# Optimization experiments

Measured on AMD Instinct MI355X. Metric: run time of the kernel, lower is better.

Reference implementation:

```python
import jax, jax.numpy as jnp
import numpy as np

B, H, S, D = 4, 16, 2048, 64
NEG = -9e15


def setup_inputs() -> dict:
    key = jax.random.key(0)
    kq, kk, kv = jax.random.split(key, 3)
    q = jax.random.normal(kq, (B, H, S, D), dtype=jnp.float32)
    k = jax.random.normal(kk, (B, H, S, D), dtype=jnp.float32)
    v = jax.random.normal(kv, (B, H, S, D), dtype=jnp.float32)
    # causal mask: 1 where attention allowed, 0 where masked
    mask = jnp.tril(jnp.ones((S, S), dtype=jnp.int32))[None, None]
    return {"q": q, "k": k, "v": v, "mask": mask}


def reference(q, k, v, mask):
    d_k = q.shape[-1]
    # [B,H,S,S] scores
    scores = jnp.einsum("bhqd,bhkd->bhqk", q, k) / jnp.sqrt(jnp.float32(d_k))
    scores = jnp.where(mask == 0, jnp.float32(NEG), scores)
    attn = jax.nn.softmax(scores, axis=-1)
    return jnp.einsum("bhqk,bhkd->bhqd", attn, v)
```

## Files before the change

kernel.cpp:

```cpp
#include <hip/hip_runtime.h>

#define SLEN 2048
#define DH 64
#define NH 64
#define KVB 64
#define NT 32
#define NP 16
#define NEGBIG (-1e30f)
#define SCALE 0.18033688011112042f

typedef __attribute__((ext_vector_type(8))) short bf16x8;
typedef __attribute__((ext_vector_type(8))) unsigned short u16x8;
typedef __attribute__((ext_vector_type(16))) float f32x16;
typedef __attribute__((ext_vector_type(4))) float f32x4;
typedef __attribute__((ext_vector_type(4))) unsigned int u32x4;

__device__ __forceinline__ ushort f2bf(float f) {
  union { float f; unsigned int u; } v; v.f = f;
  unsigned int r = v.u + 0x7fffu + ((v.u >> 16) & 1u);
  return (ushort)(r >> 16);
}

__device__ __forceinline__ unsigned int cvtpk(float lo, float hi2) {
  unsigned int r;
  asm("v_cvt_pk_bf16_f32 %0, %1, %2" : "=v"(r) : "v"(lo), "v"(hi2));
  return r;
}

__device__ __forceinline__ float xsumh(float x) { return x + __shfl_xor(x, 32); }

__device__ __forceinline__ void gload16(const ushort* g, ushort* l) {
  __builtin_amdgcn_global_load_lds(
      (const __attribute__((address_space(1))) void*)g,
      (__attribute__((address_space(3))) void*)l, 16, 0, 0);
}

__global__ __launch_bounds__(256) void prep_kv(const float* __restrict__ Kg,
                                               const float* __restrict__ Vg,
                                               ushort* __restrict__ wsK,
                                               ushort* __restrict__ wsV) {
  __shared__ float Vsh[KVB][DH + 1];
  const int head = blockIdx.x, tile = blockIdx.y, tid = threadIdx.x;
  const size_t goff = ((size_t)head * SLEN + (size_t)tile * KVB) * DH;
  const float* srcK = Kg + goff;
  const float* srcV = Vg + goff;
  ushort* dstK = wsK + ((size_t)head * NT + tile) * (KVB * DH);
  ushort* dstV = wsV + ((size_t)head * NT + tile) * (KVB * DH);
#pragma unroll
  for (int i = 0; i < 2; ++i) {
    const int id = tid + i * 256;
    const int r = id >> 3, c = id & 7;
    float4 a = *reinterpret_cast<const float4*>(srcK + r * DH + c * 8);
    float4 b = *reinterpret_cast<const float4*>(srcK + r * DH + c * 8 + 4);
    u16x8 t;
    t[0] = f2bf(a.x); t[1] = f2bf(a.y); t[2] = f2bf(a.z); t[3] = f2bf(a.w);
    t[4] = f2bf(b.x); t[5] = f2bf(b.y); t[6] = f2bf(b.z); t[7] = f2bf(b.w);
    *reinterpret_cast<u16x8*>(dstK + r * DH + ((c ^ (r & 7)) * 8)) = t;
  }
#pragma unroll
  for (int i = 0; i < 4; ++i) {
    const int n = tid + i * 256;
    const int row = n >> 4, c4 = (n & 15) << 2;
    *reinterpret_cast<float4*>(&Vsh[row][c4]) =
        *reinterpret_cast<const float4*>(srcV + row * DH + c4);
  }
  __syncthreads();
#pragma unroll
  for (int i = 0; i < 2; ++i) {
    const int id = tid + i * 256;
    const int d = id >> 3, c = id & 7;
    u16x8 t;
#pragma unroll
    for (int j = 0; j < 8; ++j) t[j] = f2bf(Vsh[c * 8 + j][d]);
    *reinterpret_cast<u16x8*>(dstV + d * DH + ((c ^ (d & 7)) * 8)) = t;
  }
}

__device__ __forceinline__ void qkt(const ushort* __restrict__ Kl,
                                    const bf16x8* qf, f32x16& s0, f32x16& s1,
                                    int ql, int hi) {
  s0 = (f32x16)0.0f; s1 = (f32x16)0.0f;
  __builtin_amdgcn_s_setprio(1);
#pragma unroll
  for (int ks = 0; ks < 4; ++ks) {
    const int c = ((ks * 2 + hi) ^ (ql & 7)) * 8;
    bf16x8 kf0 = *reinterpret_cast<const bf16x8*>(Kl + ql * 64 + c);
    bf16x8 kf1 = *reinterpret_cast<const bf16x8*>(Kl + (32 + ql) * 64 + c);
    s0 = __builtin_amdgcn_mfma_f32_32x32x16_bf16(kf0, qf[ks], s0, 0, 0, 0);
    s1 = __builtin_amdgcn_mfma_f32_32x32x16_bf16(kf1, qf[ks], s1, 0, 0, 0);
  }
  __builtin_amdgcn_s_setprio(0);
}

__device__ __forceinline__ void fin(const ushort* __restrict__ Vl,
                                    f32x16& s0, f32x16& s1, f32x16& o0,
                                    f32x16& o1, f32x4& lv, int t,
                                    int tl, int q0, int ql, int hi) {
  if (t == tl) {
    const int qg = q0 + ql;
#pragma unroll
    for (int r = 0; r < 16; ++r) {
      const int kr = t * 64 + (r & 3) + 8 * (r >> 2) + 4 * hi;
      if (kr > qg)      s0[r] = NEGBIG;
      if (kr + 32 > qg) s1[r] = NEGBIG;
    }
  }
#pragma unroll
  for (int r = 0; r < 16; ++r) s0[r] = __builtin_exp2f(s0[r]);
#pragma unroll
  for (int r = 0; r < 16; ++r) s1[r] = __builtin_exp2f(s1[r]);
#pragma unroll
  for (int r = 0; r < 16; ++r) lv[r & 3] += s0[r] + s1[r];

  unsigned int pw0[8], pw1[8];
#pragma unroll
  for (int g = 0; g < 4; ++g)
#pragma unroll
    for (int j = 0; j < 2; ++j) {
      pw0[g * 2 + j] = cvtpk(s0[4 * g + 2 * j], s0[4 * g + 2 * j + 1]);
      pw1[g * 2 + j] = cvtpk(s1[4 * g + 2 * j], s1[4 * g + 2 * j + 1]);
    }

  __builtin_amdgcn_s_setprio(1);
#pragma unroll
  for (int st = 0; st < 4; ++st) {
    const unsigned int* PW = (st < 2) ? pw0 : pw1;
    const int KH = st & 1;
    const unsigned int a0 = PW[4 * KH + 0], a1 = PW[4 * KH + 1];
    const unsigned int b0 = PW[4 * KH + 2], b1 = PW[4 * KH + 3];
    const unsigned int s0w = hi ? a0 : b0, s1w = hi ? a1 : b1;
    const unsigned int r0 = __shfl_xor(s0w, 32), r1 = __shfl_xor(s1w, 32);
    const unsigned int k0 = hi ? b0 : a0, k1 = hi ? b1 : a1;
    u32x4 fu;
    fu[0] = hi ? r0 : k0; fu[1] = hi ? r1 : k1;
    fu[2] = hi ? k0 : r0; fu[3] = hi ? k1 : r1;
    const bf16x8 pf = __builtin_bit_cast(bf16x8, fu);
    const int cv = ((st * 2 + hi) ^ (ql & 7)) * 8;
    const bf16x8 vf0 = *reinterpret_cast<const bf16x8*>(Vl + ql * 64 + cv);
    const bf16x8 vf1 = *reinterpret_cast<const bf16x8*>(Vl + (32 + ql) * 64 + cv);
    o0 = __builtin_amdgcn_mfma_f32_32x32x16_bf16(vf0, pf, o0, 0, 0, 0);
    o1 = __builtin_amdgcn_mfma_f32_32x32x16_bf16(vf1, pf, o1, 0, 0, 0);
  }
  __builtin_amdgcn_s_setprio(0);
}

__device__ __forceinline__ void load_q(const float* Qh, int q0, int ql, int hi,
                                       bf16x8* qf) {
  const float* qrow = Qh + (size_t)(q0 + ql) * DH;
#pragma unroll
  for (int ks = 0; ks < 4; ++ks) {
    const int d0 = ks * 16 + hi * 8;
    float4 a = *reinterpret_cast<const float4*>(qrow + d0);
    float4 b = *reinterpret_cast<const float4*>(qrow + d0 + 4);
    bf16x8 t;
    t[0] = (short)f2bf(a.x * SCALE); t[1] = (short)f2bf(a.y * SCALE);
    t[2] = (short)f2bf(a.z * SCALE); t[3] = (short)f2bf(a.w * SCALE);
    t[4] = (short)f2bf(b.x * SCALE); t[5] = (short)f2bf(b.y * SCALE);
    t[6] = (short)f2bf(b.z * SCALE); t[7] = (short)f2bf(b.w * SCALE);
    qf[ks] = t;
  }
}

__device__ __forceinline__ void epi(float* Ow, float* Oh, const f32x16& o,
                                    float invl, int q0, int subd, int lane) {
  const int ql = lane & 31, hi = lane >> 5;
#pragma unroll
  for (int g = 0; g < 4; ++g) {
    float4 vv = make_float4(o[4 * g] * invl, o[4 * g + 1] * invl,
                            o[4 * g + 2] * invl, o[4 * g + 3] * invl);
    *reinterpret_cast<float4*>(Ow + ql * 36 + 8 * g + 4 * hi) = vv;
  }
#pragma unroll
  for (int i = 0; i < 4; ++i) {
    const int qr = (lane >> 3) + i * 8;
    const int c4 = (lane & 7) * 4;
    float4 vv = *reinterpret_cast<const float4*>(Ow + qr * 36 + c4);
    *reinterpret_cast<float4*>(Oh + (size_t)(q0 + qr) * DH + subd * 32 + c4) = vv;
  }
}

__global__ __launch_bounds__(256, 4) void attn_fwd12(
    const float* __restrict__ Qg, const ushort* __restrict__ wsK,
    const ushort* __restrict__ wsV, float* __restrict__ Og) {
  __shared__ __align__(16) float smem[8192];
  ushort* stg = (ushort*)smem;

  const int head = blockIdx.x;
  const int p    = blockIdx.y;
  const int tid  = threadIdx.x;
  const int w    = tid >> 6;
  const int lane = tid & 63;
  const int hi   = lane >> 5;
  const int ql   = lane & 31;
  const int sel   = w & 1;
  const int which = w >> 1;

  const int q0 = (which ? (31 - p) : p) * 64 + sel * 32;
  const int tl = q0 >> 6;
  const int nt = 32 - p;

  const float*  Qh    = Qg + (size_t)head * SLEN * DH;
  float*        Oh    = Og + (size_t)head * SLEN * DH;
  const ushort* kbase = wsK + (size_t)head * (NT * KVB * DH);
  const ushort* vbase = wsV + (size_t)head * (NT * KVB * DH);

#define STAGE(buf, t)                                                          \
  do {                                                                         \
    const size_t tb_ = (size_t)(t) * 4096;                                     \
    _Pragma("unroll")                                                          \
    for (int j_ = 0; j_ < 2; ++j_) {                                           \
      gload16(kbase + tb_ + j_ * 2048 + tid * 8,                               \
              stg + (buf) * 8192 + j_ * 2048 + tid * 8);                       \
      gload16(vbase + tb_ + j_ * 2048 + tid * 8,                               \
              stg + (buf) * 8192 + 4096 + j_ * 2048 + tid * 8);                \
    }                                                                          \
  } while (0)

  STAGE(0, 0);

  bf16x8 qf[4];
  load_q(Qh, q0, ql, hi, qf);

  f32x16 o0 = (f32x16)0.0f, o1 = (f32x16)0.0f;
  f32x4 lv = (f32x4)0.0f;

  __syncthreads();

  int cur = 0;
  for (int t = 0; t < nt; ++t) {
    if (t + 1 < nt) STAGE(cur ^ 1, t + 1);

    if (t <= tl) {
      const ushort* Kl = stg + cur * 8192;
      const ushort* Vl = Kl + 4096;
      f32x16 s0, s1;
      qkt(Kl, qf, s0, s1, ql, hi);
      fin(Vl, s0, s1, o0, o1, lv, t, tl, q0, ql, hi);
    }
    __syncthreads();
    cur ^= 1;
  }
#undef STAGE

  const float ls = xsumh(lv[0] + lv[1] + lv[2] + lv[3]);

  float* Ow = smem + w * 1152;
  const float il = 1.0f / ls;
  epi(Ow, Oh, o0, il, q0, 0, lane);
  epi(Ow, Oh, o1, il, q0, 1, lane);
}

extern "C" void kernel_launch(void* const* d_in, const int* in_sizes, int n_in,
                              void* d_out, int out_size, void* d_ws, size_t ws_size,
                              hipStream_t stream) {
  const float* q = (const float*)d_in[0];
  const float* k = (const float*)d_in[1];
  const float* v = (const float*)d_in[2];
  float* out = (float*)d_out;

  const size_t per = (size_t)NH * SLEN * DH;
  ushort* wsK = (ushort*)d_ws;
  ushort* wsV = wsK + per;

  prep_kv<<<dim3(NH, NT), 256, 0, stream>>>(k, v, wsK, wsV);
  attn_fwd12<<<dim3(NH, NP), 256, 0, stream>>>(q, wsK, wsV, out);
}
```

Before: 95.74 us.

## Process two 32-row query tiles per wave to reuse K/V fragments

Each wave now handles a 64-row macro query tile (two 32-row halves), so every K and V fragment read from LDS feeds twice as many MFMAs. The grid is halved to 8 blocks per head, and each block's four waves take macro tiles b, 31-b, 8+b and 23-b, with the order reversed on odd heads to balance causal work. The goal is to cut LDS traffic and staging cost per unit of compute. In exchange, register pressure roughly doubles (launch bounds drop to 2 waves/SIMD occupancy) and the grid has fewer blocks.

```diff
diff --git a/kernel.cpp b/kernel.cpp
--- a/kernel.cpp
+++ b/kernel.cpp
@@ -5,7 +5,6 @@
 #define NH 64
 #define KVB 64
 #define NT 32
-#define NP 16
 #define NEGBIG (-1e30f)
 #define SCALE 0.18033688011112042f
 
@@ -76,72 +75,16 @@
   }
 }
 
-__device__ __forceinline__ void qkt(const ushort* __restrict__ Kl,
-                                    const bf16x8* qf, f32x16& s0, f32x16& s1,
-                                    int ql, int hi) {
-  s0 = (f32x16)0.0f; s1 = (f32x16)0.0f;
-  __builtin_amdgcn_s_setprio(1);
-#pragma unroll
-  for (int ks = 0; ks < 4; ++ks) {
-    const int c = ((ks * 2 + hi) ^ (ql & 7)) * 8;
-    bf16x8 kf0 = *reinterpret_cast<const bf16x8*>(Kl + ql * 64 + c);
-    bf16x8 kf1 = *reinterpret_cast<const bf16x8*>(Kl + (32 + ql) * 64 + c);
-    s0 = __builtin_amdgcn_mfma_f32_32x32x16_bf16(kf0, qf[ks], s0, 0, 0, 0);
-    s1 = __builtin_amdgcn_mfma_f32_32x32x16_bf16(kf1, qf[ks], s1, 0, 0, 0);
-  }
-  __builtin_amdgcn_s_setprio(0);
-}
-
-__device__ __forceinline__ void fin(const ushort* __restrict__ Vl,
-                                    f32x16& s0, f32x16& s1, f32x16& o0,
-                                    f32x16& o1, f32x4& lv, int t,
-                                    int tl, int q0, int ql, int hi) {
-  if (t == tl) {
-    const int qg = q0 + ql;
-#pragma unroll
-    for (int r = 0; r < 16; ++r) {
-      const int kr = t * 64 + (r & 3) + 8 * (r >> 2) + 4 * hi;
-      if (kr > qg)      s0[r] = NEGBIG;
-      if (kr + 32 > qg) s1[r] = NEGBIG;
-    }
-  }
-#pragma unroll
-  for (int r = 0; r < 16; ++r) s0[r] = __builtin_exp2f(s0[r]);
-#pragma unroll
-  for (int r = 0; r < 16; ++r) s1[r] = __builtin_exp2f(s1[r]);
-#pragma unroll
-  for (int r = 0; r < 16; ++r) lv[r & 3] += s0[r] + s1[r];
-
-  unsigned int pw0[8], pw1[8];
-#pragma unroll
-  for (int g = 0; g < 4; ++g)
-#pragma unroll
-    for (int j = 0; j < 2; ++j) {
-      pw0[g * 2 + j] = cvtpk(s0[4 * g + 2 * j], s0[4 * g + 2 * j + 1]);
-      pw1[g * 2 + j] = cvtpk(s1[4 * g + 2 * j], s1[4 * g + 2 * j + 1]);
-    }
-
-  __builtin_amdgcn_s_setprio(1);
-#pragma unroll
-  for (int st = 0; st < 4; ++st) {
-    const unsigned int* PW = (st < 2) ? pw0 : pw1;
-    const int KH = st & 1;
-    const unsigned int a0 = PW[4 * KH + 0], a1 = PW[4 * KH + 1];
-    const unsigned int b0 = PW[4 * KH + 2], b1 = PW[4 * KH + 3];
-    const unsigned int s0w = hi ? a0 : b0, s1w = hi ? a1 : b1;
-    const unsigned int r0 = __shfl_xor(s0w, 32), r1 = __shfl_xor(s1w, 32);
-    const unsigned int k0 = hi ? b0 : a0, k1 = hi ? b1 : a1;
-    u32x4 fu;
-    fu[0] = hi ? r0 : k0; fu[1] = hi ? r1 : k1;
-    fu[2] = hi ? k0 : r0; fu[3] = hi ? k1 : r1;
-    const bf16x8 pf = __builtin_bit_cast(bf16x8, fu);
-    const int cv = ((st * 2 + hi) ^ (ql & 7)) * 8;
-    const bf16x8 vf0 = *reinterpret_cast<const bf16x8*>(Vl + ql * 64 + cv);
-    const bf16x8 vf1 = *reinterpret_cast<const bf16x8*>(Vl + (32 + ql) * 64 + cv);
-    o0 = __builtin_amdgcn_mfma_f32_32x32x16_bf16(vf0, pf, o0, 0, 0, 0);
-    o1 = __builtin_amdgcn_mfma_f32_32x32x16_bf16(vf1, pf, o1, 0, 0, 0);
-  }
-  __builtin_amdgcn_s_setprio(0);
+__device__ __forceinline__ bf16x8 xchg(const unsigned int* PW, int KH, int hi) {
+  const unsigned int a0 = PW[4 * KH + 0], a1 = PW[4 * KH + 1];
+  const unsigned int b0 = PW[4 * KH + 2], b1 = PW[4 * KH + 3];
+  const unsigned int s0w = hi ? a0 : b0, s1w = hi ? a1 : b1;
+  const unsigned int r0 = __shfl_xor(s0w, 32), r1 = __shfl_xor(s1w, 32);
+  const unsigned int k0 = hi ? b0 : a0, k1 = hi ? b1 : a1;
+  u32x4 fu;
+  fu[0] = hi ? r0 : k0; fu[1] = hi ? r1 : k1;
+  fu[2] = hi ? k0 : r0; fu[3] = hi ? k1 : r1;
+  return __builtin_bit_cast(bf16x8, fu);
 }
 
 __device__ __forceinline__ void load_q(const float* Qh, int q0, int ql, int hi,
@@ -179,25 +122,31 @@
   }
 }
 
-__global__ __launch_bounds__(256, 4) void attn_fwd12(
+__global__ __launch_bounds__(256, 2) void attn_fwd13(
     const float* __restrict__ Qg, const ushort* __restrict__ wsK,
     const ushort* __restrict__ wsV, float* __restrict__ Og) {
   __shared__ __align__(16) float smem[8192];
   ushort* stg = (ushort*)smem;
 
   const int head = blockIdx.x;
-  const int p    = blockIdx.y;
+  const int b    = blockIdx.y;
   const int tid  = threadIdx.x;
   const int w    = tid >> 6;
   const int lane = tid & 63;
   const int hi   = lane >> 5;
   const int ql   = lane & 31;
-  const int sel   = w & 1;
-  const int which = w >> 1;
-
-  const int q0 = (which ? (31 - p) : p) * 64 + sel * 32;
-  const int tl = q0 >> 6;
-  const int nt = 32 - p;
+
+  const int wi = (head & 1) ? (3 - w) : w;
+  int macro;
+  if      (wi == 0) macro = b;
+  else if (wi == 1) macro = 31 - b;
+  else if (wi == 2) macro = 8 + b;
+  else              macro = 23 - b;
+
+  const int q0L = macro * 64;
+  const int q0U = macro * 64 + 32;
+  const int tl  = macro;
+  const int nt  = 32 - b;
 
   const float*  Qh    = Qg + (size_t)head * SLEN * DH;
   float*        Oh    = Og + (size_t)head * SLEN * DH;
@@ -218,11 +167,13 @@
 
   STAGE(0, 0);
 
-  bf16x8 qf[4];
-  load_q(Qh, q0, ql, hi, qf);
-
-  f32x16 o0 = (f32x16)0.0f, o1 = (f32x16)0.0f;
-  f32x4 lv = (f32x4)0.0f;
+  bf16x8 qfL[4], qfU[4];
+  load_q(Qh, q0L, ql, hi, qfL);
+  load_q(Qh, q0U, ql, hi, qfU);
+
+  f32x16 oL0 = (f32x16)0.0f, oL1 = (f32x16)0.0f;
+  f32x16 oU0 = (f32x16)0.0f, oU1 = (f32x16)0.0f;
+  f32x4 lvL = (f32x4)0.0f, lvU = (f32x4)0.0f;
 
   __syncthreads();
 
@@ -233,21 +184,89 @@
     if (t <= tl) {
       const ushort* Kl = stg + cur * 8192;
       const ushort* Vl = Kl + 4096;
-      f32x16 s0, s1;
-      qkt(Kl, qf, s0, s1, ql, hi);
-      fin(Vl, s0, s1, o0, o1, lv, t, tl, q0, ql, hi);
+
+      f32x16 sL0 = (f32x16)0.0f, sL1 = (f32x16)0.0f;
+      f32x16 sU0 = (f32x16)0.0f, sU1 = (f32x16)0.0f;
+      __builtin_amdgcn_s_setprio(1);
+#pragma unroll
+      for (int ks = 0; ks < 4; ++ks) {
+        const int c = ((ks * 2 + hi) ^ (ql & 7)) * 8;
+        const bf16x8 kf0 = *reinterpret_cast<const bf16x8*>(Kl + ql * 64 + c);
+        const bf16x8 kf1 =
+            *reinterpret_cast<const bf16x8*>(Kl + (32 + ql) * 64 + c);
+        sL0 = __builtin_amdgcn_mfma_f32_32x32x16_bf16(kf0, qfL[ks], sL0, 0, 0, 0);
+        sU0 = __builtin_amdgcn_mfma_f32_32x32x16_bf16(kf0, qfU[ks], sU0, 0, 0, 0);
+        sL1 = __builtin_amdgcn_mfma_f32_32x32x16_bf16(kf1, qfL[ks], sL1, 0, 0, 0);
+        sU1 = __builtin_amdgcn_mfma_f32_32x32x16_bf16(kf1, qfU[ks], sU1, 0, 0, 0);
+      }
+      __builtin_amdgcn_s_setprio(0);
+
+      if (t == tl) {
+#pragma unroll
+        for (int r = 0; r < 16; ++r) {
+          const int kr = t * 64 + (r & 3) + 8 * (r >> 2) + 4 * hi;
+          const int qgL = q0L + ql, qgU = q0U + ql;
+          if (kr > qgL)      sL0[r] = NEGBIG;
+          if (kr + 32 > qgL) sL1[r] = NEGBIG;
+          if (kr > qgU)      sU0[r] = NEGBIG;
+          if (kr + 32 > qgU) sU1[r] = NEGBIG;
+        }
+      }
+
+#pragma unroll
+      for (int r = 0; r < 16; ++r) sL0[r] = __builtin_exp2f(sL0[r]);
+#pragma unroll
+      for (int r = 0; r < 16; ++r) sL1[r] = __builtin_exp2f(sL1[r]);
+#pragma unroll
+      for (int r = 0; r < 16; ++r) sU0[r] = __builtin_exp2f(sU0[r]);
+#pragma unroll
+      for (int r = 0; r < 16; ++r) sU1[r] = __builtin_exp2f(sU1[r]);
+#pragma unroll
+      for (int r = 0; r < 16; ++r) lvL[r & 3] += sL0[r] + sL1[r];
+#pragma unroll
+      for (int r = 0; r < 16; ++r) lvU[r & 3] += sU0[r] + sU1[r];
+
+      unsigned int pwL0[8], pwL1[8], pwU0[8], pwU1[8];
+#pragma unroll
+      for (int g = 0; g < 4; ++g)
+#pragma unroll
+        for (int j = 0; j < 2; ++j) {
+          pwL0[g * 2 + j] = cvtpk(sL0[4 * g + 2 * j], sL0[4 * g + 2 * j + 1]);
+          pwL1[g * 2 + j] = cvtpk(sL1[4 * g + 2 * j], sL1[4 * g + 2 * j + 1]);
+          pwU0[g * 2 + j] = cvtpk(sU0[4 * g + 2 * j], sU0[4 * g + 2 * j + 1]);
+          pwU1[g * 2 + j] = cvtpk(sU1[4 * g + 2 * j], sU1[4 * g + 2 * j + 1]);
+        }
+
+      __builtin_amdgcn_s_setprio(1);
+#pragma unroll
+      for (int st = 0; st < 4; ++st) {
+        const int cv = ((st * 2 + hi) ^ (ql & 7)) * 8;
+        const bf16x8 vf0 = *reinterpret_cast<const bf16x8*>(Vl + ql * 64 + cv);
+        const bf16x8 vf1 =
+            *reinterpret_cast<const bf16x8*>(Vl + (32 + ql) * 64 + cv);
+        const bf16x8 pfL = xchg(st < 2 ? pwL0 : pwL1, st & 1, hi);
+        oL0 = __builtin_amdgcn_mfma_f32_32x32x16_bf16(vf0, pfL, oL0, 0, 0, 0);
+        oL1 = __builtin_amdgcn_mfma_f32_32x32x16_bf16(vf1, pfL, oL1, 0, 0, 0);
+        const bf16x8 pfU = xchg(st < 2 ? pwU0 : pwU1, st & 1, hi);
+        oU0 = __builtin_amdgcn_mfma_f32_32x32x16_bf16(vf0, pfU, oU0, 0, 0, 0);
+        oU1 = __builtin_amdgcn_mfma_f32_32x32x16_bf16(vf1, pfU, oU1, 0, 0, 0);
+      }
+      __builtin_amdgcn_s_setprio(0);
     }
     __syncthreads();
     cur ^= 1;
   }
 #undef STAGE
 
-  const float ls = xsumh(lv[0] + lv[1] + lv[2] + lv[3]);
+  const float lL = xsumh(lvL[0] + lvL[1] + lvL[2] + lvL[3]);
+  const float lU = xsumh(lvU[0] + lvU[1] + lvU[2] + lvU[3]);
 
   float* Ow = smem + w * 1152;
-  const float il = 1.0f / ls;
-  epi(Ow, Oh, o0, il, q0, 0, lane);
-  epi(Ow, Oh, o1, il, q0, 1, lane);
+  const float iL = 1.0f / lL, iU = 1.0f / lU;
+  epi(Ow, Oh, oL0, iL, q0L, 0, lane);
+  epi(Ow, Oh, oL1, iL, q0L, 1, lane);
+  epi(Ow, Oh, oU0, iU, q0U, 0, lane);
+  epi(Ow, Oh, oU1, iU, q0U, 1, lane);
 }
 
 extern "C" void kernel_launch(void* const* d_in, const int* in_sizes, int n_in,
@@ -263,5 +282,5 @@
   ushort* wsV = wsK + per;
 
   prep_kv<<<dim3(NH, NT), 256, 0, stream>>>(k, v, wsK, wsV);
-  attn_fwd12<<<dim3(NH, NP), 256, 0, stream>>>(q, wsK, wsV, out);
-}
+  attn_fwd13<<<dim3(NH, 8), 256, 0, stream>>>(q, wsK, wsV, out);
+}
```

Result: slower. 115.6 us (+20.7%).
